# Performance work log

Hardware: AMD Instinct MI355X
Metric: run time of the kernel (lower is better)

Reference implementation:

```python
import jax, jax.numpy as jnp
import numpy as np

TOP_K = 2


def setup_inputs() -> dict:
    key = jax.random.key(0)
    kx, kw = jax.random.split(key)
    x = jax.random.normal(kx, (4, 8192, 1024), dtype=jnp.float32)
    W = jax.random.normal(kw, (64, 1024), dtype=jnp.float32) * 0.02  # nn.Linear weight [E, H]
    return {"x": x, "W": W}


def reference(x, W):
    # fixed_shape_mode path of RuchbahStableMoEGate.forward
    B, S, H = x.shape
    x_flat = x.reshape(-1, H)                          # [T, H], T = B*S
    logits = jnp.einsum("th,eh->te", x_flat, W)        # gate(x_flat): [T, E]
    scores = jax.nn.softmax(logits, axis=-1)           # [T, E]
    top_scores, top_idx = jax.lax.top_k(scores, TOP_K) # [T, k], [T, k]
    # renormalize top-k scores in fp32, cast back to x dtype
    top_scores = jax.nn.softmax(top_scores.astype(jnp.float32), axis=-1).astype(x.dtype)
    return top_scores, top_idx, jnp.zeros((), dtype=x.dtype)
```

## Files before the change

### kernel.cpp

```cpp
#include <hip/hip_runtime.h>

#define H 1024
#define E 64
#define BT 64
#define BK 64

__global__ __launch_bounds__(256) void moe_gate_kernel(
    const float* __restrict__ x, const float* __restrict__ W,
    float* __restrict__ out, int T) {
  __shared__ float xs[BT][BK + 4];
  __shared__ float ws[E][BK + 4];
  float(*ls)[65] = (float(*)[65])xs;

  const int tid = threadIdx.x;
  const int tx = tid & 15;
  const int ty = tid >> 4;
  const int t0 = blockIdx.x * BT;

  float acc[4][4];
#pragma unroll
  for (int r = 0; r < 4; ++r)
#pragma unroll
    for (int c = 0; c < 4; ++c) acc[r][c] = 0.f;

  for (int k0 = 0; k0 < H; k0 += BK) {
#pragma unroll
    for (int l = 0; l < 4; ++l) {
      int id = tid + l * 256;
      int row = id >> 4;
      int c4 = id & 15;
      *(float4*)&xs[row][c4 << 2] =
          *(const float4*)&x[(size_t)(t0 + row) * H + k0 + (c4 << 2)];
      int wc = c4 ^ (row >> 2);
      *(float4*)&ws[row][wc << 2] =
          *(const float4*)&W[(size_t)row * H + k0 + (c4 << 2)];
    }
    __syncthreads();

#pragma unroll
    for (int kk = 0; kk < BK; kk += 4) {
      const int kkf = kk >> 2;
      float4 a[4], b[4];
#pragma unroll
      for (int r = 0; r < 4; ++r) a[r] = *(const float4*)&xs[ty * 4 + r][kk];
#pragma unroll
      for (int c = 0; c < 4; ++c)
        b[c] = *(const float4*)&ws[tx * 4 + c][(kkf ^ tx) << 2];
#pragma unroll
      for (int r = 0; r < 4; ++r)
#pragma unroll
        for (int c = 0; c < 4; ++c) {
          acc[r][c] += a[r].x * b[c].x;
          acc[r][c] += a[r].y * b[c].y;
          acc[r][c] += a[r].z * b[c].z;
          acc[r][c] += a[r].w * b[c].w;
        }
    }
    __syncthreads();
  }

#pragma unroll
  for (int r = 0; r < 4; ++r)
#pragma unroll
    for (int c = 0; c < 4; ++c) ls[ty * 4 + r][tx * 4 + c] = acc[r][c];
  __syncthreads();

  if (tid < BT) {
    const int tk = tid;
    float m1 = -1e30f, m2 = -1e30f;
    int i1 = 0, i2 = 0;
#pragma unroll
    for (int e = 0; e < E; ++e) {
      float v = ls[tk][e];
      if (v > m1) {
        m2 = m1; i2 = i1;
        m1 = v;  i1 = e;
      } else if (v > m2) {
        m2 = v; i2 = e;
      }
    }
    float s = 0.f;
#pragma unroll
    for (int e = 0; e < E; ++e) s += expf(ls[tk][e] - m1);
    float p1 = 1.f / s;
    float p2 = expf(m2 - m1) / s;
    float e12 = expf(p2 - p1);
    float s1 = 1.f / (1.f + e12);
    float s2 = e12 * s1;

    size_t t = (size_t)(t0 + tk);
    out[t * 2 + 0] = s1;
    out[t * 2 + 1] = s2;
    float* idxo = out + (size_t)2 * T;
    idxo[t * 2 + 0] = (float)i1;
    idxo[t * 2 + 1] = (float)i2;
  }

  if (blockIdx.x == 0 && tid == 0) out[(size_t)4 * T] = 0.f;
}

extern "C" void kernel_launch(void* const* d_in, const int* in_sizes, int n_in,
                              void* d_out, int out_size, void* d_ws, size_t ws_size,
                              hipStream_t stream) {
  const float* x = (const float*)d_in[0];
  const float* W = (const float*)d_in[1];
  float* out = (float*)d_out;
  const int T = in_sizes[0] / H;
  dim3 grid(T / BT), block(256);
  hipLaunchKernelGGL(moe_gate_kernel, grid, block, 0, stream, x, W, out, T);
}
```

Baseline: 231.0 us.

## Restructure gate GEMM: per-wave expert slices with scalar W loads and double-buffered x

```diff
diff --git a/kernel.cpp b/kernel.cpp
--- a/kernel.cpp
+++ b/kernel.cpp
@@ -4,65 +4,75 @@
 #define E 64
 #define BT 64
 #define BK 64
+#define NCH (H / BK)
+#define EPW 8
 
-__global__ __launch_bounds__(256) void moe_gate_kernel(
+__global__ __launch_bounds__(512, 4) void moe_gate_kernel(
     const float* __restrict__ x, const float* __restrict__ W,
     float* __restrict__ out, int T) {
-  __shared__ float xs[BT][BK + 4];
-  __shared__ float ws[E][BK + 4];
-  float(*ls)[65] = (float(*)[65])xs;
+  __shared__ float xs[2][BT][BK + 4];
+  float(*ls)[E + 1] = (float(*)[E + 1])xs;
 
   const int tid = threadIdx.x;
-  const int tx = tid & 15;
-  const int ty = tid >> 4;
+  const int lane = tid & 63;
+  const int wid = __builtin_amdgcn_readfirstlane(tid >> 6);
+  const int e0 = wid * EPW;
   const int t0 = blockIdx.x * BT;
 
-  float acc[4][4];
+  const int r0 = tid >> 4;
+  const int c0 = tid & 15;
+  const int r1 = r0 + 32;
+  const float* xp0 = x + (size_t)(t0 + r0) * H + (c0 << 2);
+  const float* xp1 = x + (size_t)(t0 + r1) * H + (c0 << 2);
+
+  float acc[EPW];
 #pragma unroll
-  for (int r = 0; r < 4; ++r)
+  for (int e = 0; e < EPW; ++e) acc[e] = 0.f;
+
+  {
+    float4 a = *(const float4*)xp0;
+    float4 b = *(const float4*)xp1;
+    *(float4*)&xs[0][r0][c0 << 2] = a;
+    *(float4*)&xs[0][r1][c0 << 2] = b;
+  }
+  __syncthreads();
+
+  for (int c = 0; c < NCH; ++c) {
+    const int cur = c & 1;
+    const bool more = (c + 1 < NCH);
+    float4 na{}, nb{};
+    if (more) {
+      na = *(const float4*)(xp0 + (c + 1) * BK);
+      nb = *(const float4*)(xp1 + (c + 1) * BK);
+    }
+
+    float4 xv[BK / 4];
 #pragma unroll
-    for (int c = 0; c < 4; ++c) acc[r][c] = 0.f;
+    for (int j = 0; j < BK / 4; ++j)
+      xv[j] = *(const float4*)&xs[cur][lane][j << 2];
 
-  for (int k0 = 0; k0 < H; k0 += BK) {
+    const float* Wc = W + (size_t)e0 * H + c * BK;
 #pragma unroll
-    for (int l = 0; l < 4; ++l) {
-      int id = tid + l * 256;
-      int row = id >> 4;
-      int c4 = id & 15;
-      *(float4*)&xs[row][c4 << 2] =
-          *(const float4*)&x[(size_t)(t0 + row) * H + k0 + (c4 << 2)];
-      int wc = c4 ^ (row >> 2);
-      *(float4*)&ws[row][wc << 2] =
-          *(const float4*)&W[(size_t)row * H + k0 + (c4 << 2)];
+    for (int j = 0; j < BK / 4; ++j) {
+#pragma unroll
+      for (int e = 0; e < EPW; ++e) {
+        float4 wv = *(const float4*)(Wc + (size_t)e * H + (j << 2));
+        acc[e] = fmaf(xv[j].x, wv.x, acc[e]);
+        acc[e] = fmaf(xv[j].y, wv.y, acc[e]);
+        acc[e] = fmaf(xv[j].z, wv.z, acc[e]);
+        acc[e] = fmaf(xv[j].w, wv.w, acc[e]);
+      }
     }
-    __syncthreads();
 
-#pragma unroll
-    for (int kk = 0; kk < BK; kk += 4) {
-      const int kkf = kk >> 2;
-      float4 a[4], b[4];
-#pragma unroll
-      for (int r = 0; r < 4; ++r) a[r] = *(const float4*)&xs[ty * 4 + r][kk];
-#pragma unroll
-      for (int c = 0; c < 4; ++c)
-        b[c] = *(const float4*)&ws[tx * 4 + c][(kkf ^ tx) << 2];
-#pragma unroll
-      for (int r = 0; r < 4; ++r)
-#pragma unroll
-        for (int c = 0; c < 4; ++c) {
-          acc[r][c] += a[r].x * b[c].x;
-          acc[r][c] += a[r].y * b[c].y;
-          acc[r][c] += a[r].z * b[c].z;
-          acc[r][c] += a[r].w * b[c].w;
-        }
+    if (more) {
+      *(float4*)&xs[cur ^ 1][r0][c0 << 2] = na;
+      *(float4*)&xs[cur ^ 1][r1][c0 << 2] = nb;
     }
     __syncthreads();
   }
 
 #pragma unroll
-  for (int r = 0; r < 4; ++r)
-#pragma unroll
-    for (int c = 0; c < 4; ++c) ls[ty * 4 + r][tx * 4 + c] = acc[r][c];
+  for (int e = 0; e < EPW; ++e) ls[lane][e0 + e] = acc[e];
   __syncthreads();
 
   if (tid < BT) {
@@ -106,6 +116,6 @@
   const float* W = (const float*)d_in[1];
   float* out = (float*)d_out;
   const int T = in_sizes[0] / H;
-  dim3 grid(T / BT), block(256);
+  dim3 grid(T / BT), block(512);
   hipLaunchKernelGGL(moe_gate_kernel, grid, block, 0, stream, x, W, out, T);
 }
```

Result: slower. 330.5 us (+43.1%).

## Split K across four warp groups with 8x8 register tiles and prefetch

Applied to the files above, without the earlier changes.

```diff
diff --git a/kernel.cpp b/kernel.cpp
--- a/kernel.cpp
+++ b/kernel.cpp
@@ -2,67 +2,119 @@
 
 #define H 1024
 #define E 64
-#define BT 64
-#define BK 64
+#define BT 128
+#define NG 4
+#define KG (H / NG)
+#define BK 16
+#define NCH (KG / BK)
+#define PADF 20
+#define R 8
+#define C 8
 
-__global__ __launch_bounds__(256) void moe_gate_kernel(
+typedef float __attribute__((ext_vector_type(4))) f4;
+
+__global__ __launch_bounds__(512, 2) void moe_gate_kernel(
     const float* __restrict__ x, const float* __restrict__ W,
     float* __restrict__ out, int T) {
-  __shared__ float xs[BT][BK + 4];
-  __shared__ float ws[E][BK + 4];
-  float(*ls)[65] = (float(*)[65])xs;
+  __shared__ __align__(16) float xs[NG][BT][PADF];
+  __shared__ __align__(16) float ws[NG][E][PADF];
+  float(*ls)[E + 1] = (float(*)[E + 1])xs;
 
   const int tid = threadIdx.x;
-  const int tx = tid & 15;
-  const int ty = tid >> 4;
+  const int g = __builtin_amdgcn_readfirstlane(tid >> 7);
+  const int tg = tid & 127;
+  const int tx = tg & 7;
+  const int ty = tg >> 3;
   const int t0 = blockIdx.x * BT;
+  const int kbase = g * KG;
 
-  float acc[4][4];
+  float acc[R][C];
 #pragma unroll
-  for (int r = 0; r < 4; ++r)
+  for (int r = 0; r < R; ++r)
 #pragma unroll
-    for (int c = 0; c < 4; ++c) acc[r][c] = 0.f;
+    for (int c = 0; c < C; ++c) acc[r][c] = 0.f;
 
-  for (int k0 = 0; k0 < H; k0 += BK) {
+  int xrow[4], xcol[4], wrow[2], wcol[2];
 #pragma unroll
-    for (int l = 0; l < 4; ++l) {
-      int id = tid + l * 256;
-      int row = id >> 4;
-      int c4 = id & 15;
-      *(float4*)&xs[row][c4 << 2] =
-          *(const float4*)&x[(size_t)(t0 + row) * H + k0 + (c4 << 2)];
-      int wc = c4 ^ (row >> 2);
-      *(float4*)&ws[row][wc << 2] =
-          *(const float4*)&W[(size_t)row * H + k0 + (c4 << 2)];
+  for (int k = 0; k < 4; ++k) {
+    int id = tg + (k << 7);
+    xrow[k] = id >> 2; xcol[k] = id & 3;
+  }
+#pragma unroll
+  for (int k = 0; k < 2; ++k) {
+    int id = tg + (k << 7);
+    wrow[k] = id >> 2; wcol[k] = id & 3;
+  }
+
+#pragma unroll
+  for (int k = 0; k < 4; ++k)
+    *(f4*)&xs[g][xrow[k]][xcol[k] << 2] =
+        *(const f4*)&x[(size_t)(t0 + xrow[k]) * H + kbase + (xcol[k] << 2)];
+#pragma unroll
+  for (int k = 0; k < 2; ++k)
+    *(f4*)&ws[g][wrow[k]][wcol[k] << 2] =
+        *(const f4*)&W[(size_t)wrow[k] * H + kbase + (wcol[k] << 2)];
+  __syncthreads();
+
+  for (int ch = 0; ch < NCH; ++ch) {
+    const bool more = ch + 1 < NCH;
+    f4 px[4], pw[2];
+    if (more) {
+      const int ko = kbase + (ch + 1) * BK;
+#pragma unroll
+      for (int k = 0; k < 4; ++k)
+        px[k] = *(const f4*)&x[(size_t)(t0 + xrow[k]) * H + ko + (xcol[k] << 2)];
+#pragma unroll
+      for (int k = 0; k < 2; ++k)
+        pw[k] = *(const f4*)&W[(size_t)wrow[k] * H + ko + (wcol[k] << 2)];
+    }
+
+#pragma unroll
+    for (int j = 0; j < BK / 4; ++j) {
+      f4 a[R], b[C];
+#pragma unroll
+      for (int r = 0; r < R; ++r)
+        a[r] = *(const f4*)&xs[g][ty + (r << 4)][j << 2];
+#pragma unroll
+      for (int c = 0; c < C; ++c)
+        b[c] = *(const f4*)&ws[g][tx + (c << 3)][j << 2];
+#pragma unroll
+      for (int r = 0; r < R; ++r)
+#pragma unroll
+        for (int c = 0; c < C; ++c) {
+          acc[r][c] = fmaf(a[r].x, b[c].x, acc[r][c]);
+          acc[r][c] = fmaf(a[r].y, b[c].y, acc[r][c]);
+          acc[r][c] = fmaf(a[r].z, b[c].z, acc[r][c]);
+          acc[r][c] = fmaf(a[r].w, b[c].w, acc[r][c]);
+        }
     }
     __syncthreads();
-
+    if (more) {
 #pragma unroll
-    for (int kk = 0; kk < BK; kk += 4) {
-      const int kkf = kk >> 2;
-      float4 a[4], b[4];
+      for (int k = 0; k < 4; ++k)
+        *(f4*)&xs[g][xrow[k]][xcol[k] << 2] = px[k];
 #pragma unroll
-      for (int r = 0; r < 4; ++r) a[r] = *(const float4*)&xs[ty * 4 + r][kk];
-#pragma unroll
-      for (int c = 0; c < 4; ++c)
-        b[c] = *(const float4*)&ws[tx * 4 + c][(kkf ^ tx) << 2];
-#pragma unroll
-      for (int r = 0; r < 4; ++r)
-#pragma unroll
-        for (int c = 0; c < 4; ++c) {
-          acc[r][c] += a[r].x * b[c].x;
-          acc[r][c] += a[r].y * b[c].y;
-          acc[r][c] += a[r].z * b[c].z;
-          acc[r][c] += a[r].w * b[c].w;
-        }
+      for (int k = 0; k < 2; ++k)
+        *(f4*)&ws[g][wrow[k]][wcol[k] << 2] = pw[k];
     }
     __syncthreads();
   }
 
+  if (g == 0) {
 #pragma unroll
-  for (int r = 0; r < 4; ++r)
+    for (int r = 0; r < R; ++r)
 #pragma unroll
-    for (int c = 0; c < 4; ++c) ls[ty * 4 + r][tx * 4 + c] = acc[r][c];
+      for (int c = 0; c < C; ++c)
+        ls[ty + (r << 4)][tx + (c << 3)] = acc[r][c];
+  }
+  __syncthreads();
+  if (g != 0) {
+#pragma unroll
+    for (int r = 0; r < R; ++r)
+#pragma unroll
+      for (int c = 0; c < C; ++c)
+        atomicAdd(&ls[ty + (r << 4)][tx + (c << 3)], acc[r][c]);
+  }
   __syncthreads();
 
   if (tid < BT) {
@@ -106,6 +158,6 @@
   const float* W = (const float*)d_in[1];
   float* out = (float*)d_out;
   const int T = in_sizes[0] / H;
-  dim3 grid(T / BT), block(256);
+  dim3 grid(T / BT), block(512);
   hipLaunchKernelGGL(moe_gate_kernel, grid, block, 0, stream, x, W, out, T);
 }
```

Result: slower. 612.6 us (+165.2%).
